# Kernel tuning notes

Hardware: AMD Instinct MI355X
Metric: run time of the kernel (lower is better)

The kernel has to match this reference:

```python
import jax, jax.numpy as jnp
import numpy as np
import math

N, D_MODEL, H = 2048, 1024, 16
DK = D_MODEL // H
EPS = 1e-5


def setup_inputs() -> dict:
    key = jax.random.key(0)
    ks = jax.random.split(key, 10)
    s = 0.05  # scale to keep attention logits in a sane range
    return {
        "x": jax.random.normal(ks[0], (N, D_MODEL), jnp.float32),
        "wq": jax.random.normal(ks[1], (H * D_MODEL, DK), jnp.float32) * s,
        "q_bias": jax.random.normal(ks[2], (H, DK), jnp.float32) * s,
        "wk": jax.random.normal(ks[3], (H * D_MODEL, DK), jnp.float32) * s,
        "k_bias": jax.random.normal(ks[4], (H, DK), jnp.float32) * s,
        "wv": jax.random.normal(ks[5], (H * D_MODEL, DK), jnp.float32) * s,
        "v_bias": jax.random.normal(ks[6], (H, DK), jnp.float32) * s,
        "wo": jax.random.normal(ks[7], (D_MODEL, D_MODEL), jnp.float32) * s,
        "o_bias": jax.random.normal(ks[8], (D_MODEL,), jnp.float32) * s,
        "alpha": jnp.ones((D_MODEL,), jnp.float32),
        "beta": jnp.zeros((D_MODEL,), jnp.float32),
        "n": N,
        "d_model": D_MODEL,
        "h": H,
    }


def reference(x, wq, q_bias, wk, k_bias, wv, v_bias, wo, o_bias, alpha, beta, n, d_model, h):
    dk = d_model // h
    # per-head weight slices wq[i*d_model:(i+1)*d_model] -> [h, d_model, dk]
    wq3 = wq.reshape(h, d_model, dk)
    wk3 = wk.reshape(h, d_model, dk)
    wv3 = wv.reshape(h, d_model, dk)
    q = jnp.einsum('nd,hdk->hnk', x, wq3) + q_bias[:, None, :]  # [h,n,dk]
    k = jnp.einsum('nd,hdk->hnk', x, wk3) + k_bias[:, None, :]
    v = jnp.einsum('nd,hdk->hnk', x, wv3) + v_bias[:, None, :]
    scores = jnp.einsum('hnk,hmk->hnm', q, k) / math.sqrt(dk)  # [h,n,n]
    attn = jax.nn.softmax(scores, axis=-1)  # dim=1 of 2D [n,n] == last dim
    heads = jnp.einsum('hnm,hmk->hnk', attn, v)  # [h,n,dk]
    concat = heads.transpose(1, 0, 2).reshape(n, d_model)  # [n, d_model]
    out = concat @ wo + o_bias + x  # out-proj + residual
    mu = jnp.mean(out, axis=-1, keepdims=True)
    var = jnp.mean(jnp.square(out - mu), axis=-1, keepdims=True)
    return alpha * (out - mu) / jnp.sqrt(var + EPS) + beta
```

## Files before the change

### kernel.cpp

```cpp
#include <hip/hip_runtime.h>


#define NN 2048
#define DM 1024
#define NH 16
#define DKH 64

typedef __attribute__((ext_vector_type(4))) float f32x4;
typedef __attribute__((ext_vector_type(8))) __bf16 bf16x8;
typedef __attribute__((ext_vector_type(4))) __bf16 bf16x4;

#define AS1 __attribute__((address_space(1)))
#define AS3 __attribute__((address_space(3)))
#define GLOAD16(g, l) __builtin_amdgcn_global_load_lds((const AS1 void*)(g), (AS3 void*)(l), 16, 0, 0)

static __device__ __forceinline__ f32x4 mfma16(bf16x8 a, bf16x8 b, f32x4 c) {
  return __builtin_amdgcn_mfma_f32_16x16x32_bf16(a, b, c, 0, 0, 0);
}


__global__ __launch_bounds__(256) void cvt_x(const float* __restrict__ in,
                                             __bf16* __restrict__ out) {
  int i = (blockIdx.x * 256 + threadIdx.x) * 8;
  float4 a = *(const float4*)(in + i);
  float4 b = *(const float4*)(in + i + 4);
  bf16x8 o;
  o[0] = (__bf16)a.x; o[1] = (__bf16)a.y; o[2] = (__bf16)a.z; o[3] = (__bf16)a.w;
  o[4] = (__bf16)b.x; o[5] = (__bf16)b.y; o[6] = (__bf16)b.z; o[7] = (__bf16)b.w;
  *(bf16x8*)(out + i) = o;
}

__global__ __launch_bounds__(256) void cvt_wqkv(const float* __restrict__ wq,
                                                const float* __restrict__ wk,
                                                const float* __restrict__ wv,
                                                __bf16* __restrict__ out) {
  int c = blockIdx.x * 256 + threadIdx.x;
  int oct = blockIdx.y;
  const float* src = (c < 1024) ? wq : (c < 2048 ? wk : wv);
  int hk = c & 1023;
  int hh = hk >> 6, dkk = hk & 63;
  bf16x8 o;
#pragma unroll
  for (int j = 0; j < 8; ++j)
    o[j] = (__bf16)src[(hh * 1024 + oct * 8 + j) * 64 + dkk];
  *(bf16x8*)(out + c * 1024 + oct * 8) = o;
}

__global__ __launch_bounds__(256) void cvt_wo(const float* __restrict__ wo,
                                              __bf16* __restrict__ out) {
  int c = blockIdx.x * 256 + threadIdx.x;
  int oct = blockIdx.y;
  bf16x8 o;
#pragma unroll
  for (int j = 0; j < 8; ++j)
    o[j] = (__bf16)wo[(oct * 8 + j) * 1024 + c];
  *(bf16x8*)(out + c * 1024 + oct * 8) = o;
}

__global__ __launch_bounds__(256) void gemm_qkv(const __bf16* __restrict__ A,
                                                const __bf16* __restrict__ Bt,
                                                const float* __restrict__ biasq,
                                                const float* __restrict__ biask,
                                                const float* __restrict__ biasv,
                                                __bf16* __restrict__ Qo,
                                                __bf16* __restrict__ Ko,
                                                __bf16* __restrict__ Vto) {
  __shared__ __align__(16) __bf16 Al[2][128 * 32];
  __shared__ __align__(16) __bf16 Bl[2][128 * 32];
  const int t = threadIdx.x;
  const int w = t >> 6, lane = t & 63, l15 = lane & 15, g = lane >> 4;
  const int m0 = blockIdx.y * 128, n0 = blockIdx.x * 128;
  const int wr = (w >> 1) * 64, wc = (w & 1) * 64;

  f32x4 acc[4][4] = {};

#define STAGE_QKV(buf, k0v)                                                      \
  do {                                                                           \
    _Pragma("unroll") for (int i = 0; i < 2; ++i) {                              \
      int L = (w * 2 + i) * 64 + lane;                                           \
      int row = L >> 2, kc = L & 3;                                              \
      GLOAD16(A + (m0 + row) * DM + (k0v) + kc * 8,                              \
              (char*)Al + (buf) * 8192 + (w * 2 + i) * 1024);                    \
      GLOAD16(Bt + (n0 + row) * DM + (k0v) + kc * 8,                             \
              (char*)Bl + (buf) * 8192 + (w * 2 + i) * 1024);                    \
    }                                                                            \
  } while (0)

  STAGE_QKV(0, 0);
  __syncthreads();
  int cur = 0;
  for (int k0 = 0; k0 < DM; k0 += 32) {
    if (k0 + 32 < DM) STAGE_QKV(cur ^ 1, k0 + 32);
    const char* Ab = (const char*)Al + cur * 8192;
    const char* Bb = (const char*)Bl + cur * 8192;
    bf16x8 af[4], bfv[4];
#pragma unroll
    for (int mf = 0; mf < 4; ++mf)
      af[mf] = *(const bf16x8*)(Ab + (wr + mf * 16 + l15) * 64 + g * 16);
#pragma unroll
    for (int nf = 0; nf < 4; ++nf)
      bfv[nf] = *(const bf16x8*)(Bb + (wc + nf * 16 + l15) * 64 + g * 16);
#pragma unroll
    for (int mf = 0; mf < 4; ++mf)
#pragma unroll
      for (int nf = 0; nf < 4; ++nf)
        acc[mf][nf] = mfma16(af[mf], bfv[nf], acc[mf][nf]);
    __syncthreads();
    cur ^= 1;
  }

  const int mtx = n0 >> 10;
  if (mtx == 0) {
#pragma unroll
    for (int nf = 0; nf < 4; ++nf) {
      int hk = (n0 & 1023) + wc + nf * 16 + l15;
      int hh = hk >> 6, dkk = hk & 63;
      float bias = biasq[hk];
#pragma unroll
      for (int mf = 0; mf < 4; ++mf)
#pragma unroll
        for (int r = 0; r < 4; ++r) {
          int n = m0 + wr + mf * 16 + g * 4 + r;
          Qo[(hh * NN + n) * DKH + dkk] = (__bf16)((acc[mf][nf][r] + bias) * 0.18033688f);
        }
    }
  } else if (mtx == 1) {
#pragma unroll
    for (int nf = 0; nf < 4; ++nf) {
      int hk = (n0 & 1023) + wc + nf * 16 + l15;
      int hh = hk >> 6, dkk = hk & 63;
      float bias = biask[hk];
#pragma unroll
      for (int mf = 0; mf < 4; ++mf)
#pragma unroll
        for (int r = 0; r < 4; ++r) {
          int n = m0 + wr + mf * 16 + g * 4 + r;
          Ko[(hh * NN + n) * DKH + dkk] = (__bf16)(acc[mf][nf][r] + bias);
        }
    }
  } else {
#pragma unroll
    for (int nf = 0; nf < 4; ++nf) {
      int hk = (n0 & 1023) + wc + nf * 16 + l15;
      int hh = hk >> 6, dkk = hk & 63;
      float bias = biasv[hk];
#pragma unroll
      for (int mf = 0; mf < 4; ++mf) {
        int nb = m0 + wr + mf * 16 + g * 4;
        bf16x4 pk;
#pragma unroll
        for (int r = 0; r < 4; ++r) pk[r] = (__bf16)(acc[mf][nf][r] + bias);
        *(bf16x4*)(Vto + hh * (DKH * NN) + dkk * NN + nb) = pk;
      }
    }
  }
}

__global__ __launch_bounds__(256) void attn_kernel(const __bf16* __restrict__ Qg,
                                                   const __bf16* __restrict__ Kg,
                                                   const __bf16* __restrict__ Vtg,
                                                   __bf16* __restrict__ Og) {
  __shared__ __align__(16) char Kl[2][8192];
  __shared__ __align__(16) char Vl[2][8192];
  __shared__ __align__(16) char Pl[4][2304];
  const int t = threadIdx.x;
  const int w = t >> 6, lane = t & 63, l15 = lane & 15, g = lane >> 4;
  const int h = blockIdx.y;
  const int qb0 = blockIdx.x * 64;
  const int swz = (l15 & 7) << 4;

  const __bf16* qptr = Qg + (h * NN + qb0 + w * 16 + l15) * DKH + g * 8;
  bf16x8 qf0 = *(const bf16x8*)qptr;
  bf16x8 qf1 = *(const bf16x8*)(qptr + 32);

  bf16x8 vones;
#pragma unroll
  for (int j = 0; j < 8; ++j) vones[j] = (__bf16)1.0f;

  f32x4 oacc[4] = {};
  f32x4 lacc = {};

#define STAGE_ATTN(buf, kbv)                                                     \
  do {                                                                           \
    _Pragma("unroll") for (int i = 0; i < 2; ++i) {                              \
      int L = w * 128 + i * 64 + lane;                                           \
      int rowi = L >> 3;                                                         \
      int kc = (L & 7) ^ (rowi & 7);                                             \
      GLOAD16(Kg + (h * NN + (kbv) + rowi) * DKH + kc * 8,                       \
              Kl[buf] + w * 2048 + i * 1024);                                    \
      GLOAD16(Vtg + h * (DKH * NN) + rowi * NN + (kbv) + kc * 8,                 \
              Vl[buf] + w * 2048 + i * 1024);                                    \
    }                                                                            \
  } while (0)

  STAGE_ATTN(0, 0);
  __syncthreads();
  int cur = 0;
  for (int kb = 0; kb < NN; kb += 64) {
    if (kb + 64 < NN) STAGE_ATTN(cur ^ 1, kb + 64);

    f32x4 s[4];
#pragma unroll
    for (int h2 = 0; h2 < 4; ++h2) {
      bf16x8 kf0 = *(const bf16x8*)(Kl[cur] + ((((h2 * 16 + l15) * 128) + g * 16) ^ swz));
      bf16x8 kf1 = *(const bf16x8*)(Kl[cur] + ((((h2 * 16 + l15) * 128) + 64 + g * 16) ^ swz));
      f32x4 z = {};
      z = mfma16(qf0, kf0, z);
      z = mfma16(qf1, kf1, z);
      s[h2] = z;
    }

#pragma unroll
    for (int h2 = 0; h2 < 4; ++h2)
#pragma unroll
      for (int r = 0; r < 4; ++r)
        *(__bf16*)(Pl[w] + (g * 4 + r) * 144 + (h2 * 16 + l15) * 2) =
            (__bf16)exp2f(s[h2][r]);

#pragma unroll
    for (int ks = 0; ks < 2; ++ks) {
      bf16x8 pa = *(const bf16x8*)(Pl[w] + l15 * 144 + ks * 64 + g * 16);
#pragma unroll
      for (int cb = 0; cb < 4; ++cb) {
        bf16x8 vf = *(const bf16x8*)(Vl[cur] + ((((cb * 16 + l15) * 128) + ks * 64 + g * 16) ^ swz));
        oacc[cb] = mfma16(pa, vf, oacc[cb]);
      }
      lacc = mfma16(pa, vones, lacc);
    }
    __syncthreads();
    cur ^= 1;
  }

#pragma unroll
  for (int r = 0; r < 4; ++r) {
    float inv = 1.0f / lacc[r];
    int q = qb0 + w * 16 + g * 4 + r;
#pragma unroll
    for (int cb = 0; cb < 4; ++cb)
      Og[q * DM + h * DKH + cb * 16 + l15] = (__bf16)(oacc[cb][r] * inv);
  }
}

__global__ __launch_bounds__(256) void gemm_proj(const __bf16* __restrict__ A,
                                                 const __bf16* __restrict__ Bt,
                                                 const float* __restrict__ obias,
                                                 const float* __restrict__ xres,
                                                 float* __restrict__ outp) {
  __shared__ __align__(16) __bf16 Al[2][128 * 32];
  __shared__ __align__(16) __bf16 Bl[2][64 * 32];
  const int t = threadIdx.x;
  const int w = t >> 6, lane = t & 63, l15 = lane & 15, g = lane >> 4;
  const int m0 = blockIdx.y * 128, n0 = blockIdx.x * 64;

  f32x4 acc[2][4] = {};

#define STAGE_PROJ(buf, k0v)                                                     \
  do {                                                                           \
    _Pragma("unroll") for (int i = 0; i < 2; ++i) {                              \
      int L = (w * 2 + i) * 64 + lane;                                           \
      int row = L >> 2, kc = L & 3;                                              \
      GLOAD16(A + (m0 + row) * DM + (k0v) + kc * 8,                              \
              (char*)Al + (buf) * 8192 + (w * 2 + i) * 1024);                    \
    }                                                                            \
    {                                                                            \
      int L = w * 64 + lane;                                                     \
      int row = L >> 2, kc = L & 3;                                              \
      GLOAD16(Bt + (n0 + row) * DM + (k0v) + kc * 8,                             \
              (char*)Bl + (buf) * 4096 + w * 1024);                              \
    }                                                                            \
  } while (0)

  STAGE_PROJ(0, 0);
  __syncthreads();
  int cur = 0;
  for (int k0 = 0; k0 < DM; k0 += 32) {
    if (k0 + 32 < DM) STAGE_PROJ(cur ^ 1, k0 + 32);
    const char* Ab = (const char*)Al + cur * 8192;
    const char* Bb = (const char*)Bl + cur * 4096;
    bf16x8 af[2], bfv[4];
#pragma unroll
    for (int mf = 0; mf < 2; ++mf)
      af[mf] = *(const bf16x8*)(Ab + (w * 32 + mf * 16 + l15) * 64 + g * 16);
#pragma unroll
    for (int nf = 0; nf < 4; ++nf)
      bfv[nf] = *(const bf16x8*)(Bb + (nf * 16 + l15) * 64 + g * 16);
#pragma unroll
    for (int mf = 0; mf < 2; ++mf)
#pragma unroll
      for (int nf = 0; nf < 4; ++nf)
        acc[mf][nf] = mfma16(af[mf], bfv[nf], acc[mf][nf]);
    __syncthreads();
    cur ^= 1;
  }

#pragma unroll
  for (int nf = 0; nf < 4; ++nf) {
    int col = n0 + nf * 16 + l15;
    float ob = obias[col];
#pragma unroll
    for (int mf = 0; mf < 2; ++mf)
#pragma unroll
      for (int r = 0; r < 4; ++r) {
        int row = m0 + w * 32 + mf * 16 + g * 4 + r;
        outp[row * DM + col] = acc[mf][nf][r] + ob + xres[row * DM + col];
      }
  }
}

__global__ __launch_bounds__(256) void ln_kernel(const float* __restrict__ in,
                                                 const float* __restrict__ alpha,
                                                 const float* __restrict__ beta,
                                                 float* __restrict__ out) {
  const int row = blockIdx.x, t = threadIdx.x;
  const int lane = t & 63, w = t >> 6;
  float4 v = ((const float4*)(in + row * DM))[t];
  float s = v.x + v.y + v.z + v.w;
  float s2 = v.x * v.x + v.y * v.y + v.z * v.z + v.w * v.w;
#pragma unroll
  for (int off = 32; off >= 1; off >>= 1) {
    s += __shfl_xor(s, off);
    s2 += __shfl_xor(s2, off);
  }
  __shared__ float ps[8];
  if (lane == 0) { ps[w] = s; ps[4 + w] = s2; }
  __syncthreads();
  float S = ps[0] + ps[1] + ps[2] + ps[3];
  float S2 = ps[4] + ps[5] + ps[6] + ps[7];
  float mu = S * (1.0f / DM);
  float var = S2 * (1.0f / DM) - mu * mu;
  float rstd = rsqrtf(var + 1e-5f);
  float4 a = ((const float4*)alpha)[t];
  float4 b = ((const float4*)beta)[t];
  float4 o;
  o.x = a.x * (v.x - mu) * rstd + b.x;
  o.y = a.y * (v.y - mu) * rstd + b.y;
  o.z = a.z * (v.z - mu) * rstd + b.z;
  o.w = a.w * (v.w - mu) * rstd + b.w;
  ((float4*)(out + row * DM))[t] = o;
}

extern "C" void kernel_launch(void* const* d_in, const int* in_sizes, int n_in,
                              void* d_out, int out_size, void* d_ws, size_t ws_size,
                              hipStream_t stream) {
  const float* x     = (const float*)d_in[0];
  const float* wq    = (const float*)d_in[1];
  const float* qb    = (const float*)d_in[2];
  const float* wk    = (const float*)d_in[3];
  const float* kb    = (const float*)d_in[4];
  const float* wv    = (const float*)d_in[5];
  const float* vb    = (const float*)d_in[6];
  const float* wo    = (const float*)d_in[7];
  const float* ob    = (const float*)d_in[8];
  const float* alpha = (const float*)d_in[9];
  const float* beta  = (const float*)d_in[10];
  float* out = (float*)d_out;
  char* ws = (char*)d_ws;

  __bf16* x_bf   = (__bf16*)(ws);
  __bf16* wqkv_t = (__bf16*)(ws + (4ull << 20));
  __bf16* wo_t   = (__bf16*)(ws + (10ull << 20));
  __bf16* Qb     = (__bf16*)(ws + (12ull << 20));
  __bf16* Kb     = (__bf16*)(ws + (16ull << 20));
  __bf16* Vtb    = (__bf16*)(ws + (20ull << 20));
  __bf16* attn   = (__bf16*)(ws + (24ull << 20));
  float*  outp   = (float*)(ws + (28ull << 20));

  cvt_x<<<dim3(1024), dim3(256), 0, stream>>>(x, x_bf);
  cvt_wqkv<<<dim3(12, 128), dim3(256), 0, stream>>>(wq, wk, wv, wqkv_t);
  cvt_wo<<<dim3(4, 128), dim3(256), 0, stream>>>(wo, wo_t);
  gemm_qkv<<<dim3(24, 16), dim3(256), 0, stream>>>(x_bf, wqkv_t, qb, kb, vb, Qb, Kb, Vtb);
  attn_kernel<<<dim3(32, 16), dim3(256), 0, stream>>>(Qb, Kb, Vtb, attn);
  gemm_proj<<<dim3(16, 16), dim3(256), 0, stream>>>(attn, wo_t, ob, x, outp);
  ln_kernel<<<dim3(2048), dim3(256), 0, stream>>>(outp, alpha, beta, out);
}
```

Measured before the change: 195.0 us.

## Merge conversion kernels, remap GEMM blocks, restructure attention to 128-row register tiles

The three fp32-to-bf16 conversion kernels become one launch. Both GEMMs get a remapped 1D grid so neighbouring blocks share tiles and distribute across XCDs. The attention kernel now handles 128 queries per block in two 16-row halves per wave over 128-key tiles. It keeps P in registers instead of round-tripping through LDS, and sums the softmax denominator in scalars with lane shuffles instead of an extra MFMA. The V layout is permuted at the QKV epilogue so its rows match the register P fragments, at the cost of higher register and LDS use (launch_bounds 256,1) and fewer attention blocks.

```diff
diff --git a/kernel.cpp b/kernel.cpp
--- a/kernel.cpp
+++ b/kernel.cpp
@@ -18,43 +18,52 @@
   return __builtin_amdgcn_mfma_f32_16x16x32_bf16(a, b, c, 0, 0, 0);
 }
 
-
-__global__ __launch_bounds__(256) void cvt_x(const float* __restrict__ in,
-                                             __bf16* __restrict__ out) {
-  int i = (blockIdx.x * 256 + threadIdx.x) * 8;
-  float4 a = *(const float4*)(in + i);
-  float4 b = *(const float4*)(in + i + 4);
-  bf16x8 o;
-  o[0] = (__bf16)a.x; o[1] = (__bf16)a.y; o[2] = (__bf16)a.z; o[3] = (__bf16)a.w;
-  o[4] = (__bf16)b.x; o[5] = (__bf16)b.y; o[6] = (__bf16)b.z; o[7] = (__bf16)b.w;
-  *(bf16x8*)(out + i) = o;
-}
-
-__global__ __launch_bounds__(256) void cvt_wqkv(const float* __restrict__ wq,
-                                                const float* __restrict__ wk,
-                                                const float* __restrict__ wv,
-                                                __bf16* __restrict__ out) {
-  int c = blockIdx.x * 256 + threadIdx.x;
-  int oct = blockIdx.y;
-  const float* src = (c < 1024) ? wq : (c < 2048 ? wk : wv);
-  int hk = c & 1023;
-  int hh = hk >> 6, dkk = hk & 63;
-  bf16x8 o;
-#pragma unroll
-  for (int j = 0; j < 8; ++j)
-    o[j] = (__bf16)src[(hh * 1024 + oct * 8 + j) * 64 + dkk];
-  *(bf16x8*)(out + c * 1024 + oct * 8) = o;
-}
-
-__global__ __launch_bounds__(256) void cvt_wo(const float* __restrict__ wo,
-                                              __bf16* __restrict__ out) {
-  int c = blockIdx.x * 256 + threadIdx.x;
-  int oct = blockIdx.y;
-  bf16x8 o;
-#pragma unroll
-  for (int j = 0; j < 8; ++j)
-    o[j] = (__bf16)wo[(oct * 8 + j) * 1024 + c];
-  *(bf16x8*)(out + c * 1024 + oct * 8) = o;
+static __device__ __forceinline__ bf16x8 cat44(bf16x4 a, bf16x4 b) {
+  bf16x8 r;
+  r[0] = a[0]; r[1] = a[1]; r[2] = a[2]; r[3] = a[3];
+  r[4] = b[0]; r[5] = b[1]; r[6] = b[2]; r[7] = b[3];
+  return r;
+}
+
+__global__ __launch_bounds__(256) void cvt_all(const float* __restrict__ x,
+                                               const float* __restrict__ wq,
+                                               const float* __restrict__ wk,
+                                               const float* __restrict__ wv,
+                                               const float* __restrict__ wo,
+                                               __bf16* __restrict__ x_bf,
+                                               __bf16* __restrict__ wqkv_t,
+                                               __bf16* __restrict__ wo_t) {
+  const int b = blockIdx.x, t = threadIdx.x;
+  if (b < 1024) {
+    int i = (b * 256 + t) * 8;
+    float4 a = *(const float4*)(x + i);
+    float4 c = *(const float4*)(x + i + 4);
+    bf16x8 o;
+    o[0] = (__bf16)a.x; o[1] = (__bf16)a.y; o[2] = (__bf16)a.z; o[3] = (__bf16)a.w;
+    o[4] = (__bf16)c.x; o[5] = (__bf16)c.y; o[6] = (__bf16)c.z; o[7] = (__bf16)c.w;
+    *(bf16x8*)(x_bf + i) = o;
+  } else if (b < 2560) {
+    int bb = b - 1024;
+    int c = (bb % 12) * 256 + t;
+    int oct = bb / 12;
+    const float* src = (c < 1024) ? wq : (c < 2048 ? wk : wv);
+    int hk = c & 1023;
+    int hh = hk >> 6, dkk = hk & 63;
+    bf16x8 o;
+#pragma unroll
+    for (int j = 0; j < 8; ++j)
+      o[j] = (__bf16)src[(hh * 1024 + oct * 8 + j) * 64 + dkk];
+    *(bf16x8*)(wqkv_t + c * 1024 + oct * 8) = o;
+  } else {
+    int bb = b - 2560;
+    int c = (bb % 4) * 256 + t;
+    int oct = bb / 4;
+    bf16x8 o;
+#pragma unroll
+    for (int j = 0; j < 8; ++j)
+      o[j] = (__bf16)wo[(oct * 8 + j) * 1024 + c];
+    *(bf16x8*)(wo_t + c * 1024 + oct * 8) = o;
+  }
 }
 
 __global__ __launch_bounds__(256) void gemm_qkv(const __bf16* __restrict__ A,
@@ -69,7 +78,11 @@
   __shared__ __align__(16) __bf16 Bl[2][128 * 32];
   const int t = threadIdx.x;
   const int w = t >> 6, lane = t & 63, l15 = lane & 15, g = lane >> 4;
-  const int m0 = blockIdx.y * 128, n0 = blockIdx.x * 128;
+  const int bb = blockIdx.x;
+  const int xk = bb & 7, s = bb >> 3;
+  const int bx = (xk & 3) * 6 + s % 6;
+  const int by = (xk >> 2) * 8 + s / 6;
+  const int m0 = by * 128, n0 = bx * 128;
   const int wr = (w >> 1) * 64, wc = (w & 1) * 64;
 
   f32x4 acc[4][4] = {};
@@ -147,97 +160,113 @@
 #pragma unroll
       for (int mf = 0; mf < 4; ++mf) {
         int nb = m0 + wr + mf * 16 + g * 4;
+        int bl = nb & 127;
+        int pcol = (nb & ~127) + ((bl >> 5) << 5) + (((bl >> 2) & 3) << 3) +
+                   (((bl >> 4) & 1) << 2);
         bf16x4 pk;
 #pragma unroll
         for (int r = 0; r < 4; ++r) pk[r] = (__bf16)(acc[mf][nf][r] + bias);
-        *(bf16x4*)(Vto + hh * (DKH * NN) + dkk * NN + nb) = pk;
+        *(bf16x4*)(Vto + hh * (DKH * NN) + dkk * NN + pcol) = pk;
       }
     }
   }
 }
 
-__global__ __launch_bounds__(256) void attn_kernel(const __bf16* __restrict__ Qg,
-                                                   const __bf16* __restrict__ Kg,
-                                                   const __bf16* __restrict__ Vtg,
-                                                   __bf16* __restrict__ Og) {
-  __shared__ __align__(16) char Kl[2][8192];
-  __shared__ __align__(16) char Vl[2][8192];
-  __shared__ __align__(16) char Pl[4][2304];
+__global__ __launch_bounds__(256, 1) void attn_kernel(const __bf16* __restrict__ Qg,
+                                                      const __bf16* __restrict__ Kg,
+                                                      const __bf16* __restrict__ Vtg,
+                                                      __bf16* __restrict__ Og) {
+  __shared__ __align__(16) char Kl[2][16384];
+  __shared__ __align__(16) char Vl[2][16384];
   const int t = threadIdx.x;
   const int w = t >> 6, lane = t & 63, l15 = lane & 15, g = lane >> 4;
-  const int h = blockIdx.y;
-  const int qb0 = blockIdx.x * 64;
-  const int swz = (l15 & 7) << 4;
-
-  const __bf16* qptr = Qg + (h * NN + qb0 + w * 16 + l15) * DKH + g * 8;
-  bf16x8 qf0 = *(const bf16x8*)qptr;
-  bf16x8 qf1 = *(const bf16x8*)(qptr + 32);
-
-  bf16x8 vones;
-#pragma unroll
-  for (int j = 0; j < 8; ++j) vones[j] = (__bf16)1.0f;
-
-  f32x4 oacc[4] = {};
-  f32x4 lacc = {};
+  const int b = blockIdx.x;
+  const int h = (b & 7) * 2 + ((b >> 3) >> 4);
+  const int qb0 = ((b >> 3) & 15) * 128;
+
+  const int rA = qb0 + w * 32 + l15;
+  const __bf16* qpA = Qg + (h * NN + rA) * DKH + g * 8;
+  bf16x8 qfA0 = *(const bf16x8*)qpA;
+  bf16x8 qfA1 = *(const bf16x8*)(qpA + 32);
+  const __bf16* qpB = qpA + 16 * DKH;
+  bf16x8 qfB0 = *(const bf16x8*)qpB;
+  bf16x8 qfB1 = *(const bf16x8*)(qpB + 32);
+
+  f32x4 oaccA[4] = {}, oaccB[4] = {};
+  float lsA = 0.f, lsB = 0.f;
 
 #define STAGE_ATTN(buf, kbv)                                                     \
   do {                                                                           \
-    _Pragma("unroll") for (int i = 0; i < 2; ++i) {                              \
-      int L = w * 128 + i * 64 + lane;                                           \
-      int rowi = L >> 3;                                                         \
-      int kc = (L & 7) ^ (rowi & 7);                                             \
-      GLOAD16(Kg + (h * NN + (kbv) + rowi) * DKH + kc * 8,                       \
-              Kl[buf] + w * 2048 + i * 1024);                                    \
-      GLOAD16(Vtg + h * (DKH * NN) + rowi * NN + (kbv) + kc * 8,                 \
-              Vl[buf] + w * 2048 + i * 1024);                                    \
+    _Pragma("unroll") for (int i = 0; i < 4; ++i) {                              \
+      int L = i * 256 + t;                                                       \
+      int rk = L >> 3, ok = (L & 7) ^ (rk & 7);                                  \
+      GLOAD16(Kg + (h * NN + (kbv) + rk) * DKH + ok * 8, Kl[buf] + L * 16);      \
+    }                                                                            \
+    _Pragma("unroll") for (int i = 0; i < 4; ++i) {                              \
+      int L = i * 256 + t;                                                       \
+      int rv = L >> 4, ov = (L & 15) ^ (rv & 7);                                 \
+      GLOAD16(Vtg + h * (DKH * NN) + rv * NN + (kbv) + ov * 8, Vl[buf] + L * 16);\
     }                                                                            \
   } while (0)
 
   STAGE_ATTN(0, 0);
   __syncthreads();
   int cur = 0;
-  for (int kb = 0; kb < NN; kb += 64) {
-    if (kb + 64 < NN) STAGE_ATTN(cur ^ 1, kb + 64);
-
-    f32x4 s[4];
-#pragma unroll
-    for (int h2 = 0; h2 < 4; ++h2) {
-      bf16x8 kf0 = *(const bf16x8*)(Kl[cur] + ((((h2 * 16 + l15) * 128) + g * 16) ^ swz));
-      bf16x8 kf1 = *(const bf16x8*)(Kl[cur] + ((((h2 * 16 + l15) * 128) + 64 + g * 16) ^ swz));
-      f32x4 z = {};
-      z = mfma16(qf0, kf0, z);
-      z = mfma16(qf1, kf1, z);
-      s[h2] = z;
-    }
-
-#pragma unroll
-    for (int h2 = 0; h2 < 4; ++h2)
-#pragma unroll
-      for (int r = 0; r < 4; ++r)
-        *(__bf16*)(Pl[w] + (g * 4 + r) * 144 + (h2 * 16 + l15) * 2) =
-            (__bf16)exp2f(s[h2][r]);
-
-#pragma unroll
-    for (int ks = 0; ks < 2; ++ks) {
-      bf16x8 pa = *(const bf16x8*)(Pl[w] + l15 * 144 + ks * 64 + g * 16);
+  const int swz = (l15 & 7) << 4;
+  for (int kb = 0; kb < NN; kb += 128) {
+    if (kb + 128 < NN) STAGE_ATTN(cur ^ 1, kb + 128);
+
+    bf16x4 pkA[8], pkB[8];
+#pragma unroll
+    for (int h2 = 0; h2 < 8; ++h2) {
+      const char* kbase = Kl[cur] + (h2 * 16 + l15) * 128;
+      bf16x8 kf0 = *(const bf16x8*)(kbase + ((g * 16) ^ swz));
+      bf16x8 kf1 = *(const bf16x8*)(kbase + ((64 + g * 16) ^ swz));
+      f32x4 zA = {};
+      zA = mfma16(kf0, qfA0, zA);
+      zA = mfma16(kf1, qfA1, zA);
+      f32x4 zB = {};
+      zB = mfma16(kf0, qfB0, zB);
+      zB = mfma16(kf1, qfB1, zB);
+      float a0 = exp2f(zA[0]), a1 = exp2f(zA[1]), a2 = exp2f(zA[2]), a3 = exp2f(zA[3]);
+      lsA += (a0 + a1) + (a2 + a3);
+      pkA[h2][0] = (__bf16)a0; pkA[h2][1] = (__bf16)a1;
+      pkA[h2][2] = (__bf16)a2; pkA[h2][3] = (__bf16)a3;
+      float b0 = exp2f(zB[0]), b1 = exp2f(zB[1]), b2 = exp2f(zB[2]), b3 = exp2f(zB[3]);
+      lsB += (b0 + b1) + (b2 + b3);
+      pkB[h2][0] = (__bf16)b0; pkB[h2][1] = (__bf16)b1;
+      pkB[h2][2] = (__bf16)b2; pkB[h2][3] = (__bf16)b3;
+    }
+
+#pragma unroll
+    for (int hp = 0; hp < 4; ++hp) {
+      bf16x8 paA = cat44(pkA[2 * hp], pkA[2 * hp + 1]);
+      bf16x8 paB = cat44(pkB[2 * hp], pkB[2 * hp + 1]);
 #pragma unroll
       for (int cb = 0; cb < 4; ++cb) {
-        bf16x8 vf = *(const bf16x8*)(Vl[cur] + ((((cb * 16 + l15) * 128) + ks * 64 + g * 16) ^ swz));
-        oacc[cb] = mfma16(pa, vf, oacc[cb]);
+        int vrow = cb * 16 + l15;
+        bf16x8 vv = *(const bf16x8*)(Vl[cur] + vrow * 256 +
+                                     ((((4 * hp + g) ^ (vrow & 7))) << 4));
+        oaccA[cb] = mfma16(paA, vv, oaccA[cb]);
+        oaccB[cb] = mfma16(paB, vv, oaccB[cb]);
       }
-      lacc = mfma16(pa, vones, lacc);
     }
     __syncthreads();
     cur ^= 1;
   }
 
+  float lrA = lsA; lrA += __shfl_xor(lrA, 16); lrA += __shfl_xor(lrA, 32);
+  float lrB = lsB; lrB += __shfl_xor(lrB, 16); lrB += __shfl_xor(lrB, 32);
 #pragma unroll
   for (int r = 0; r < 4; ++r) {
-    float inv = 1.0f / lacc[r];
-    int q = qb0 + w * 16 + g * 4 + r;
-#pragma unroll
-    for (int cb = 0; cb < 4; ++cb)
-      Og[q * DM + h * DKH + cb * 16 + l15] = (__bf16)(oacc[cb][r] * inv);
+    float invA = 1.0f / __shfl(lrA, g * 4 + r);
+    float invB = 1.0f / __shfl(lrB, g * 4 + r);
+    int qA = qb0 + w * 32 + g * 4 + r;
+#pragma unroll
+    for (int cb = 0; cb < 4; ++cb) {
+      Og[qA * DM + h * DKH + cb * 16 + l15] = (__bf16)(oaccA[cb][r] * invA);
+      Og[(qA + 16) * DM + h * DKH + cb * 16 + l15] = (__bf16)(oaccB[cb][r] * invB);
+    }
   }
 }
 
@@ -250,7 +279,11 @@
   __shared__ __align__(16) __bf16 Bl[2][64 * 32];
   const int t = threadIdx.x;
   const int w = t >> 6, lane = t & 63, l15 = lane & 15, g = lane >> 4;
-  const int m0 = blockIdx.y * 128, n0 = blockIdx.x * 64;
+  const int bb = blockIdx.x;
+  const int xk = bb & 7, s = bb >> 3;
+  const int bx = (xk & 3) * 4 + (s & 3);
+  const int by = (xk >> 2) * 8 + (s >> 2);
+  const int m0 = by * 128, n0 = bx * 64;
 
   f32x4 acc[2][4] = {};
 
@@ -365,11 +398,9 @@
   __bf16* attn   = (__bf16*)(ws + (24ull << 20));
   float*  outp   = (float*)(ws + (28ull << 20));
 
-  cvt_x<<<dim3(1024), dim3(256), 0, stream>>>(x, x_bf);
-  cvt_wqkv<<<dim3(12, 128), dim3(256), 0, stream>>>(wq, wk, wv, wqkv_t);
-  cvt_wo<<<dim3(4, 128), dim3(256), 0, stream>>>(wo, wo_t);
-  gemm_qkv<<<dim3(24, 16), dim3(256), 0, stream>>>(x_bf, wqkv_t, qb, kb, vb, Qb, Kb, Vtb);
-  attn_kernel<<<dim3(32, 16), dim3(256), 0, stream>>>(Qb, Kb, Vtb, attn);
-  gemm_proj<<<dim3(16, 16), dim3(256), 0, stream>>>(attn, wo_t, ob, x, outp);
+  cvt_all<<<dim3(3072), dim3(256), 0, stream>>>(x, wq, wk, wv, wo, x_bf, wqkv_t, wo_t);
+  gemm_qkv<<<dim3(384), dim3(256), 0, stream>>>(x_bf, wqkv_t, qb, kb, vb, Qb, Kb, Vtb);
+  attn_kernel<<<dim3(256), dim3(256), 0, stream>>>(Qb, Kb, Vtb, attn);
+  gemm_proj<<<dim3(256), dim3(256), 0, stream>>>(attn, wo_t, ob, x, outp);
   ln_kernel<<<dim3(2048), dim3(256), 0, stream>>>(outp, alpha, beta, out);
 }
```

After: 184.4 us. -5.5%, faster.
